# Performance work log

Measured on AMD Instinct MI355X. Metric: run time of the kernel, lower is better.

Reference implementation:

```python
import jax, jax.numpy as jnp
import numpy as np

B, N, H, L = 8, 256, 128, 3
NF, EF, TD, FH = 6, 15, 4, 64  # node feat, edge feat, temporal dim, flow hidden


def setup_inputs() -> dict:
    key = jax.random.key(0)
    ks = jax.random.split(key, 16)
    s = 0.05
    return {
        "node_features": jax.random.normal(ks[0], (B, N, NF), jnp.float32),
        "edge_features": jax.random.normal(ks[1], (B, N, N, EF), jnp.float32),
        "temporal_features": jax.random.normal(ks[2], (B, N, N, TD), jnp.float32),
        "adjacency": jax.random.randint(ks[3], (N, N), 0, 2, jnp.int32),
        "W_emb": jax.random.normal(ks[4], (NF, H), jnp.float32) * s,
        "b_emb": jnp.zeros((H,), jnp.float32),
        "msg_W": jax.random.normal(ks[5], (L, H + 3, H), jnp.float32) * s,
        "msg_b": jnp.zeros((L, H), jnp.float32),
        "upd_W": jax.random.normal(ks[6], (L, 2 * H, H), jnp.float32) * s,
        "upd_b": jnp.zeros((L, H), jnp.float32),
        "W1": jax.random.normal(ks[7], (2 * H + 3 + TD, FH), jnp.float32) * s,
        "b1": jnp.zeros((FH,), jnp.float32),
        "W2": jax.random.normal(ks[8], (FH, 1), jnp.float32) * s,
        "b2": jnp.zeros((1,), jnp.float32),
    }


def reference(node_features, edge_features, temporal_features, adjacency,
              W_emb, b_emb, msg_W, msg_b, upd_W, upd_b, W1, b1, W2, b2):
    # mask[j, i] = 1 if node i is a neighbor of node j (adjacency[j] > 0)
    mask = (adjacency > 0).astype(node_features.dtype)          # [N, N]
    deg = mask.sum(axis=1)                                      # [N]
    edge_rel = edge_features[..., -3:]                          # [B, N, N, 3]
    # aggregated relation features per destination j: sum_i mask[j,i] * edge_rel[b,i,j,:]
    r_agg = jnp.einsum('ji,bijc->bjc', mask, edge_rel)          # [B, N, 3]

    # node embedding (dropout = identity in eval)
    emb = jax.nn.relu(node_features @ W_emb + b_emb)            # [B, N, H]

    for l in range(L):
        We, Wr = msg_W[l, :H], msg_W[l, H:]                     # [H,H], [3,H]
        # msg_nn is linear, so the masked sum decomposes exactly:
        # messages[b,j] = sum_i mask[j,i]*(emb_i @ We + r_ij @ Wr + b)
        messages = (jnp.einsum('ji,bih->bjh', mask, emb @ We)
                    + r_agg @ Wr
                    + deg[None, :, None] * msg_b[l])            # [B, N, H]
        emb = jax.nn.relu(
            jnp.concatenate([emb, messages], axis=-1) @ upd_W[l] + upd_b[l])

    # pairwise flow MLP, first Linear split by input blocks [emb_i, emb_j, r, t]
    Wi, Wj = W1[:H], W1[H:2 * H]
    Wr1, Wt = W1[2 * H:2 * H + 3], W1[2 * H + 3:]
    hi = emb @ Wi                                               # [B, N, FH]
    hj = emb @ Wj                                               # [B, N, FH]
    h = jax.nn.relu(hi[:, :, None, :] + hj[:, None, :, :]
                    + edge_rel @ Wr1 + temporal_features @ Wt + b1)  # [B,N,N,FH]
    flows = jax.nn.relu(h @ W2 + b2)[..., 0]                    # [B, N, N]
    return flows
```

## Files before the change

kernel.cpp:

```cpp
#include <hip/hip_runtime.h>

#define B 8
#define N 256
#define H 128
#define NF 6
#define EF 15
#define TD 4
#define FH 64
#define M (B*N)

typedef unsigned short u16;
using short8  = __attribute__((ext_vector_type(8))) short;
using short4v = __attribute__((ext_vector_type(4))) short;
using f32x4   = __attribute__((ext_vector_type(4))) float;

__device__ __forceinline__ u16 f2bf(float x) {
    unsigned u = __float_as_uint(x);
    u += 0x7fffu + ((u >> 16) & 1u);
    return (u16)(u >> 16);
}
__device__ __forceinline__ float bf2f(u16 h) {
    return __uint_as_float(((unsigned)h) << 16);
}

__global__ __launch_bounds__(256) void k_setup(
    const float* __restrict__ edge, const int* __restrict__ adj,
    const float* __restrict__ nf, const float* __restrict__ Wemb,
    const float* __restrict__ bemb,
    const float* __restrict__ msg_W, const float* __restrict__ upd_W,
    const float* __restrict__ W1,
    float* __restrict__ e0p, float* __restrict__ e1p, float* __restrict__ e2p,
    float* __restrict__ rp0, float* __restrict__ rp1, float* __restrict__ rp2,
    float* __restrict__ deg,
    u16* __restrict__ WeTh, u16* __restrict__ WeTl,
    u16* __restrict__ UwTh, u16* __restrict__ UwTl,
    u16* __restrict__ W1Th, u16* __restrict__ W1Tl,
    u16* __restrict__ eRh, u16* __restrict__ eRl,
    u16* __restrict__ eTh, u16* __restrict__ eTl)
{
    __shared__ __align__(16) float smem[3848];
    __shared__ float red[4];
    const int t = threadIdx.x;
    const int blk = blockIdx.x;

    if (blk < 2048) {
        const int i = blk & 255;
        const float* src = edge + (size_t)blk * (N * EF);
        float4* s4 = (float4*)smem;
#pragma unroll
        for (int u = 0; u < 4; ++u) {
            int idx = t + u * 256;
            if (idx < (N * EF) / 4) s4[idx] = *(const float4*)(src + idx * 4);
        }
        __syncthreads();
        const int j = t;
        float e0 = smem[j * EF + 12];
        float e1 = smem[j * EF + 13];
        float e2 = smem[j * EF + 14];
        size_t base = (size_t)blk * N + j;
        e0p[base] = e0; e1p[base] = e1; e2p[base] = e2;
        float m = (adj[j * N + i] > 0) ? 1.f : 0.f;
        rp0[base] = m * e0; rp1[base] = m * e1; rp2[base] = m * e2;
    } else if (blk < 2688) {
        int idx = (blk - 2048) * 256 + t;
        float v; u16 *dh, *dl; int d;
        if (idx < 3 * 16384) {
            int l = idx / 16384, r = idx & 16383;
            int c = r >> 7, h = r & 127;
            v = msg_W[l * ((H + 3) * H) + h * H + c];
            dh = WeTh; dl = WeTl; d = idx;
        } else if (idx < 3 * 16384 + 3 * 32768) {
            int r0 = idx - 3 * 16384;
            int l = r0 / 32768, r = r0 & 32767;
            int c = r >> 8, k = r & 255;
            v = upd_W[l * (2 * H * H) + k * H + c];
            dh = UwTh; dl = UwTl; d = r0;
        } else {
            int r0 = idx - 3 * 16384 - 3 * 32768;
            int f = r0 >> 8, k = r0 & 255;
            v = W1[k * FH + f];
            dh = W1Th; dl = W1Tl; d = r0;
        }
        u16 h = f2bf(v);
        dh[d] = h;
        dl[d] = f2bf(v - bf2f(h));
    } else if (blk < 2816) {
        int tile = blk - 2688;
        float (*sout)[132] = (float(*)[132])smem;
        {
            int row = t >> 4, h0 = (t & 15) * 8;
            int gr = tile * 16 + row;
            float xv[NF];
#pragma unroll
            for (int k = 0; k < NF; ++k) xv[k] = nf[gr * NF + k];
#pragma unroll
            for (int c = 0; c < 8; ++c) {
                float a = bemb[h0 + c];
#pragma unroll
                for (int k = 0; k < NF; ++k) a += xv[k] * Wemb[k * H + h0 + c];
                sout[row][h0 + c] = fmaxf(a, 0.f);
            }
        }
        __syncthreads();
        {
            int row = t >> 4, h0 = (t & 15) * 8;
            int gr = tile * 16 + row;
            short8 ph, pl;
#pragma unroll
            for (int c = 0; c < 8; ++c) {
                float x = sout[row][h0 + c];
                u16 h = f2bf(x);
                ph[c] = (short)h;
                pl[c] = (short)f2bf(x - bf2f(h));
            }
            *(short8*)&eRh[(size_t)gr * H + h0] = ph;
            *(short8*)&eRl[(size_t)gr * H + h0] = pl;
        }
        {
            int hh = t >> 1, jj = (t & 1) * 8;
            short8 th, tl;
#pragma unroll
            for (int r = 0; r < 8; ++r) {
                float x = sout[jj + r][hh];
                u16 h = f2bf(x);
                th[r] = (short)h;
                tl[r] = (short)f2bf(x - bf2f(h));
            }
            size_t o = (size_t)(tile >> 4) * H * N + (size_t)hh * N + ((tile & 15) * 16) + jj;
            *(short8*)&eTh[o] = th;
            *(short8*)&eTl[o] = tl;
        }
    } else {
        int jr = blk - 2816;
        float v = (adj[jr * N + t] > 0) ? 1.f : 0.f;
        for (int o = 32; o > 0; o >>= 1) v += __shfl_down(v, o);
        if ((t & 63) == 0) red[t >> 6] = v;
        __syncthreads();
        if (t == 0) deg[jr] = red[0] + red[1] + red[2] + red[3];
    }
}

#define PIPE(NC, LD, COMP)                          \
    LD(0, pA0, pA1);                                \
    LD(1, pB0, pB1);                                \
    WRX(0, pA0, pA1);                               \
    __syncthreads();                                \
    _Pragma("unroll")                               \
    for (int c = 0; c < (NC); c += 2) {             \
        WRX(1, pB0, pB1);                           \
        if (c + 2 < (NC)) LD(c + 2, pA0, pA1);      \
        COMP(c, 0);                                 \
        __syncthreads();                            \
        if (c + 2 < (NC)) WRX(0, pA0, pA1);         \
        if (c + 3 < (NC)) LD(c + 3, pB0, pB1);      \
        COMP(c + 1, 1);                             \
        __syncthreads();                            \
    }

template <bool FIRST, bool LAST>
__global__ __launch_bounds__(512) void k_layer(
    const u16* __restrict__ embR_hi, const u16* __restrict__ embR_lo,
    const u16* __restrict__ embT_hi, const u16* __restrict__ embT_lo,
    const int* __restrict__ adj,
    const float* __restrict__ rp0, const float* __restrict__ rp1,
    const float* __restrict__ rp2, float* __restrict__ ragg,
    const float* __restrict__ deg,
    const u16* __restrict__ WeT_hi, const u16* __restrict__ WeT_lo,
    const float* __restrict__ mwl, const float* __restrict__ mbl,
    const u16* __restrict__ UwT_hi, const u16* __restrict__ UwT_lo,
    const float* __restrict__ ubl,
    u16* __restrict__ oR_hi, u16* __restrict__ oR_lo,
    u16* __restrict__ oT_hi, u16* __restrict__ oT_lo,
    const u16* __restrict__ W1T_hi, const u16* __restrict__ W1T_lo,
    float* __restrict__ hi_out, float* __restrict__ hj_out)
{
    __shared__ __align__(16) u16 sbt[2][2][128][40];
    __shared__ __align__(16) u16 smask[16][264];
    __shared__ __align__(16) u16 semb_hi[16][136], semb_lo[16][136];
    __shared__ __align__(16) u16 sagg_hi[16][136], sagg_lo[16][136];
    __shared__ __align__(16) u16 smsg_hi[16][136], smsg_lo[16][136];
    __shared__ __align__(16) float sout[16][132];
    __shared__ float sragg[16][4];

    const int t = threadIdx.x;
    const int wave = t >> 6, lane = t & 63;
    const int lrow = lane & 15;
    const int kg8  = (lane >> 4) * 8;
    const int rb   = (lane >> 4) * 4;
    const int cb   = wave * 16;
    const int blk  = blockIdx.x;
    const int b    = blk >> 4, tile = blk & 15;
    const int j0   = tile * 16;
    const int gb   = b * N;

    const int sp = t >> 8, task = t & 255;
    const int sh = task >> 2, sseg = (task & 3) * 8;

    short8 pA0, pA1, pB0, pB1;

    {
        int j = t >> 5, i0 = (t & 31) * 8;
        int4 a0 = *(const int4*)(adj + (j0 + j) * N + i0);
        int4 a1 = *(const int4*)(adj + (j0 + j) * N + i0 + 4);
        short8 mrow;
        mrow[0] = (a0.x > 0) ? (short)0x3F80 : (short)0;
        mrow[1] = (a0.y > 0) ? (short)0x3F80 : (short)0;
        mrow[2] = (a0.z > 0) ? (short)0x3F80 : (short)0;
        mrow[3] = (a0.w > 0) ? (short)0x3F80 : (short)0;
        mrow[4] = (a1.x > 0) ? (short)0x3F80 : (short)0;
        mrow[5] = (a1.y > 0) ? (short)0x3F80 : (short)0;
        mrow[6] = (a1.z > 0) ? (short)0x3F80 : (short)0;
        mrow[7] = (a1.w > 0) ? (short)0x3F80 : (short)0;
        *(short8*)&smask[j][i0] = mrow;
        int h0 = (t & 31) * 4;
        *(short4v*)&semb_hi[j][h0] = *(const short4v*)&embR_hi[(size_t)(gb + j0 + j) * H + h0];
        *(short4v*)&semb_lo[j][h0] = *(const short4v*)&embR_lo[(size_t)(gb + j0 + j) * H + h0];
    }

    if constexpr (FIRST) {
        int j16 = t >> 5, ic = t & 31;
        int gj = gb + j0 + j16;
        float s0 = 0.f, s1 = 0.f, s2 = 0.f;
#pragma unroll
        for (int k = 0; k < 8; ++k) {
            size_t o = ((size_t)(gb + ic * 8 + k)) * N + (j0 + j16);
            s0 += rp0[o]; s1 += rp1[o]; s2 += rp2[o];
        }
        for (int o = 16; o > 0; o >>= 1) {
            s0 += __shfl_down(s0, o, 32);
            s1 += __shfl_down(s1, o, 32);
            s2 += __shfl_down(s2, o, 32);
        }
        if (ic == 0) {
            sragg[j16][0] = s0; sragg[j16][1] = s1; sragg[j16][2] = s2;
            float* rg = ragg + (size_t)gj * 3;
            rg[0] = s0; rg[1] = s1; rg[2] = s2;
        }
    } else {
        if (t < 48) sragg[t / 3][t % 3] = ragg[(size_t)(gb + j0 + t / 3) * 3 + (t % 3)];
    }

    const u16* sA_hi = embT_hi + (size_t)b * H * N;
    const u16* sA_lo = embT_lo + (size_t)b * H * N;

#define WRX(buf, q0, q1)                              \
    { *(short8*)&sbt[buf][sp][sh][sseg] = q0;         \
      *(short8*)&sbt[buf][sp][sh + 64][sseg] = q1; }

#define LDA(c, q0, q1)                                                        \
    { const u16* s_ = sp ? sA_lo : sA_hi;                                     \
      q0 = *(const short8*)(s_ + (size_t)sh * N + (c) * 32 + sseg);           \
      q1 = *(const short8*)(s_ + (size_t)(sh + 64) * N + (c) * 32 + sseg); }

#define LDB(c, q0, q1)                                                        \
    { const u16* s_ = sp ? WeT_lo : WeT_hi;                                   \
      q0 = *(const short8*)(s_ + (size_t)sh * H + (c) * 32 + sseg);           \
      q1 = *(const short8*)(s_ + (size_t)(sh + 64) * H + (c) * 32 + sseg); }

#define LDC(c, q0, q1)                                                        \
    { const u16* s_ = sp ? UwT_lo : UwT_hi;                                   \
      q0 = *(const short8*)(s_ + (size_t)sh * 2 * H + (c) * 32 + sseg);       \
      q1 = *(const short8*)(s_ + (size_t)(sh + 64) * 2 * H + (c) * 32 + sseg); }

#define LDD(c, q0, q1)                                                        \
    { const u16* s_ = sp ? W1T_lo : W1T_hi;                                   \
      q0 = *(const short8*)(s_ + (size_t)sh * 256 + (c) * 32 + sseg);         \
      q1 = *(const short8*)(s_ + (size_t)sh * 256 + 128 + (c) * 32 + sseg); }

#define COMPA(c, buf)                                                           \
    { short8 am = *(const short8*)&smask[lrow][(c) * 32 + kg8];                 \
      short8 bh = *(const short8*)&sbt[buf][0][cb + lrow][kg8];                 \
      short8 bl = *(const short8*)&sbt[buf][1][cb + lrow][kg8];                 \
      acc = __builtin_amdgcn_mfma_f32_16x16x32_bf16(am, bh, acc, 0, 0, 0);      \
      acc = __builtin_amdgcn_mfma_f32_16x16x32_bf16(am, bl, acc, 0, 0, 0); }

#define COMPB(c, buf)                                                           \
    { short8 ah = *(const short8*)&sagg_hi[lrow][(c) * 32 + kg8];               \
      short8 al = *(const short8*)&sagg_lo[lrow][(c) * 32 + kg8];               \
      short8 bh = *(const short8*)&sbt[buf][0][cb + lrow][kg8];                 \
      short8 bl = *(const short8*)&sbt[buf][1][cb + lrow][kg8];                 \
      acc = __builtin_amdgcn_mfma_f32_16x16x32_bf16(ah, bh, acc, 0, 0, 0);      \
      acc = __builtin_amdgcn_mfma_f32_16x16x32_bf16(ah, bl, acc, 0, 0, 0);      \
      acc = __builtin_amdgcn_mfma_f32_16x16x32_bf16(al, bh, acc, 0, 0, 0); }

#define COMPC(c, buf)                                                           \
    { int kc = ((c) & 3) * 32 + kg8; short8 ah, al;                             \
      if ((c) < 4) { ah = *(const short8*)&semb_hi[lrow][kc];                   \
                     al = *(const short8*)&semb_lo[lrow][kc]; }                 \
      else         { ah = *(const short8*)&smsg_hi[lrow][kc];                   \
                     al = *(const short8*)&smsg_lo[lrow][kc]; }                 \
      short8 bh = *(const short8*)&sbt[buf][0][cb + lrow][kg8];                 \
      short8 bl = *(const short8*)&sbt[buf][1][cb + lrow][kg8];                 \
      acc = __builtin_amdgcn_mfma_f32_16x16x32_bf16(ah, bh, acc, 0, 0, 0);      \
      acc = __builtin_amdgcn_mfma_f32_16x16x32_bf16(ah, bl, acc, 0, 0, 0);      \
      acc = __builtin_amdgcn_mfma_f32_16x16x32_bf16(al, bh, acc, 0, 0, 0); }

#define COMPD(c, buf)                                                           \
    { short8 ah = *(const short8*)&sagg_hi[lrow][(c) * 32 + kg8];               \
      short8 al = *(const short8*)&sagg_lo[lrow][(c) * 32 + kg8];               \
      short8 bh = *(const short8*)&sbt[buf][0][br][kg8];                        \
      short8 bl = *(const short8*)&sbt[buf][1][br][kg8];                        \
      acc = __builtin_amdgcn_mfma_f32_16x16x32_bf16(ah, bh, acc, 0, 0, 0);      \
      acc = __builtin_amdgcn_mfma_f32_16x16x32_bf16(ah, bl, acc, 0, 0, 0);      \
      acc = __builtin_amdgcn_mfma_f32_16x16x32_bf16(al, bh, acc, 0, 0, 0); }

    f32x4 acc = {0.f, 0.f, 0.f, 0.f};
    PIPE(8, LDA, COMPA)
#pragma unroll
    for (int r = 0; r < 4; ++r) {
        float v = acc[r];
        u16 h = f2bf(v);
        sagg_hi[rb + r][cb + lrow] = h;
        sagg_lo[rb + r][cb + lrow] = f2bf(v - bf2f(h));
    }

    acc = (f32x4){0.f, 0.f, 0.f, 0.f};
    PIPE(4, LDB, COMPB)
    {
        int hp = cb + lrow;
        float w0 = mwl[(H + 0) * H + hp];
        float w1 = mwl[(H + 1) * H + hp];
        float w2 = mwl[(H + 2) * H + hp];
        float mb = mbl[hp];
#pragma unroll
        for (int r = 0; r < 4; ++r) {
            int jl = j0 + rb + r;
            float v = acc[r] + deg[jl] * mb
                    + sragg[rb + r][0] * w0 + sragg[rb + r][1] * w1
                    + sragg[rb + r][2] * w2;
            u16 h = f2bf(v);
            smsg_hi[rb + r][hp] = h;
            smsg_lo[rb + r][hp] = f2bf(v - bf2f(h));
        }
    }

    acc = (f32x4){0.f, 0.f, 0.f, 0.f};
    PIPE(8, LDC, COMPC)
    {
        float ub = ubl[cb + lrow];
#pragma unroll
        for (int r = 0; r < 4; ++r) {
            float v = fmaxf(acc[r] + ub, 0.f);
            if constexpr (LAST) {
                u16 h = f2bf(v);
                sagg_hi[rb + r][cb + lrow] = h;
                sagg_lo[rb + r][cb + lrow] = f2bf(v - bf2f(h));
            } else {
                sout[rb + r][cb + lrow] = v;
            }
        }
    }
    __syncthreads();

    if constexpr (!LAST) {
        {
            int row = t >> 5, h0 = (t & 31) * 4;
            int gr = gb + j0 + row;
            float4 v = *(const float4*)&sout[row][h0];
            float xs[4] = {v.x, v.y, v.z, v.w};
            short4v ph, pl;
#pragma unroll
            for (int c = 0; c < 4; ++c) {
                u16 h = f2bf(xs[c]);
                ph[c] = (short)h;
                pl[c] = (short)f2bf(xs[c] - bf2f(h));
            }
            *(short4v*)&oR_hi[(size_t)gr * H + h0] = ph;
            *(short4v*)&oR_lo[(size_t)gr * H + h0] = pl;
        }
        {
            int hh = t >> 2, jj = (t & 3) * 4;
            short4v th, tl;
#pragma unroll
            for (int r = 0; r < 4; ++r) {
                float x = sout[jj + r][hh];
                u16 h = f2bf(x);
                th[r] = (short)h;
                tl[r] = (short)f2bf(x - bf2f(h));
            }
            size_t o = (size_t)b * H * N + (size_t)hh * N + j0 + jj;
            *(short4v*)&oT_hi[o] = th;
            *(short4v*)&oT_lo[o] = tl;
        }
    } else {
        const int br = ((wave >= 4) ? 64 : 0) + (wave & 3) * 16 + lrow;
        acc = (f32x4){0.f, 0.f, 0.f, 0.f};
        PIPE(4, LDD, COMPD)
#pragma unroll
        for (int r = 0; r < 4; ++r) sout[rb + r][br] = acc[r];
        __syncthreads();
        int row = t >> 5, c0 = (t & 31) * 4;
        int gr = gb + j0 + row;
        float4 v = *(const float4*)&sout[row][c0];
        if (c0 < 64) *(float4*)&hi_out[(size_t)gr * FH + c0] = v;
        else         *(float4*)&hj_out[(size_t)gr * FH + (c0 - 64)] = v;
    }
#undef WRX
#undef LDA
#undef LDB
#undef LDC
#undef LDD
#undef COMPA
#undef COMPB
#undef COMPC
#undef COMPD
}

__global__ __launch_bounds__(256) void k_final(
    const float* __restrict__ hi, const float* __restrict__ hj,
    const float* __restrict__ e0p, const float* __restrict__ e1p,
    const float* __restrict__ e2p, const float* __restrict__ temporal,
    const float* __restrict__ W1, const float* __restrict__ b1,
    const float* __restrict__ W2, const float* __restrict__ b2,
    float* __restrict__ flows) {
    __shared__ float his[8][FH];
    __shared__ float hjs[32][FH + 2];
    __shared__ float wr0[FH], wr1[FH], wr2[FH];
    __shared__ float wt0[FH], wt1[FH], wt2[FH], wt3[FH], bb[FH], w2s[FH];
    int blk = blockIdx.x;
    int jt = blk & 7, it = (blk >> 3) & 31, b = blk >> 8;
    int tid = threadIdx.x;
#pragma unroll
    for (int u = 0; u < 2; ++u) {
        int idx = u * 256 + tid;
        his[idx >> 6][idx & 63] = hi[((size_t)(b * N) + it * 8 + (idx >> 6)) * FH + (idx & 63)];
    }
#pragma unroll
    for (int u = 0; u < 8; ++u) {
        int idx = u * 256 + tid;
        hjs[idx >> 6][idx & 63] = hj[((size_t)(b * N) + jt * 32 + (idx >> 6)) * FH + (idx & 63)];
    }
    {
        int f = tid & 63, g = tid >> 6;
        if (g == 0) { wr0[f] = W1[(2 * H + 0) * FH + f]; wt0[f] = W1[(2 * H + 3) * FH + f]; bb[f] = b1[f]; }
        if (g == 1) { wr1[f] = W1[(2 * H + 1) * FH + f]; wt1[f] = W1[(2 * H + 4) * FH + f]; w2s[f] = W2[f]; }
        if (g == 2) { wr2[f] = W1[(2 * H + 2) * FH + f]; wt2[f] = W1[(2 * H + 5) * FH + f]; }
        if (g == 3) { wt3[f] = W1[(2 * H + 6) * FH + f]; }
    }
    __syncthreads();
    int ti = tid >> 5, tj = tid & 31;
    int i = it * 8 + ti, j = jt * 32 + tj;
    size_t pij = ((size_t)(b * N) + i) * N + j;
    float e0 = e0p[pij], e1 = e1p[pij], e2 = e2p[pij];
    float4 tf = *(const float4*)(temporal + pij * TD);
    float acc = 0.f;
#pragma unroll 8
    for (int f = 0; f < FH; ++f) {
        float v = his[ti][f] + hjs[tj][f] + bb[f]
                + e0 * wr0[f] + e1 * wr1[f] + e2 * wr2[f]
                + tf.x * wt0[f] + tf.y * wt1[f] + tf.z * wt2[f] + tf.w * wt3[f];
        acc += fmaxf(v, 0.f) * w2s[f];
    }
    flows[pij] = fmaxf(acc + b2[0], 0.f);
}

extern "C" void kernel_launch(void* const* d_in, const int* in_sizes, int n_in,
                              void* d_out, int out_size, void* d_ws, size_t ws_size,
                              hipStream_t stream) {
    const float* nf       = (const float*)d_in[0];
    const float* edge     = (const float*)d_in[1];
    const float* temporal = (const float*)d_in[2];
    const int*   adj      = (const int*)d_in[3];
    const float* W_emb    = (const float*)d_in[4];
    const float* b_emb    = (const float*)d_in[5];
    const float* msg_W    = (const float*)d_in[6];
    const float* msg_b    = (const float*)d_in[7];
    const float* upd_W    = (const float*)d_in[8];
    const float* upd_b    = (const float*)d_in[9];
    const float* W1       = (const float*)d_in[10];
    const float* b1       = (const float*)d_in[11];
    const float* W2       = (const float*)d_in[12];
    const float* b2       = (const float*)d_in[13];
    float* out = (float*)d_out;
    (void)in_sizes; (void)n_in; (void)out_size; (void)ws_size;

    char* p = (char*)d_ws;
    auto take = [&](size_t bytes) { char* r = p; p += (bytes + 255) & ~(size_t)255; return r; };
    float* deg   = (float*)take(256 * 4);
    float* ragg  = (float*)take((size_t)M * 3 * 4);
    float* e0p   = (float*)take((size_t)B * N * N * 4);
    float* e1p   = (float*)take((size_t)B * N * N * 4);
    float* e2p   = (float*)take((size_t)B * N * N * 4);
    float* rp0   = (float*)take((size_t)B * N * N * 4);
    float* rp1   = (float*)take((size_t)B * N * N * 4);
    float* rp2   = (float*)take((size_t)B * N * N * 4);
    float* hi    = (float*)take((size_t)M * FH * 4);
    float* hj    = (float*)take((size_t)M * FH * 4);
    u16* eRhA = (u16*)take((size_t)M * H * 2);
    u16* eRlA = (u16*)take((size_t)M * H * 2);
    u16* eThA = (u16*)take((size_t)M * H * 2);
    u16* eTlA = (u16*)take((size_t)M * H * 2);
    u16* eRhB = (u16*)take((size_t)M * H * 2);
    u16* eRlB = (u16*)take((size_t)M * H * 2);
    u16* eThB = (u16*)take((size_t)M * H * 2);
    u16* eTlB = (u16*)take((size_t)M * H * 2);
    u16* WeTh = (u16*)take(3 * 16384 * 2);
    u16* WeTl = (u16*)take(3 * 16384 * 2);
    u16* UwTh = (u16*)take(3 * 32768 * 2);
    u16* UwTl = (u16*)take(3 * 32768 * 2);
    u16* W1Th = (u16*)take(16384 * 2);
    u16* W1Tl = (u16*)take(16384 * 2);

    k_setup<<<3072, 256, 0, stream>>>(edge, adj, nf, W_emb, b_emb,
                                      msg_W, upd_W, W1,
                                      e0p, e1p, e2p, rp0, rp1, rp2, deg,
                                      WeTh, WeTl, UwTh, UwTl, W1Th, W1Tl,
                                      eRhA, eRlA, eThA, eTlA);

    const int mwS = (H + 3) * H;
    k_layer<true, false><<<128, 512, 0, stream>>>(
        eRhA, eRlA, eThA, eTlA, adj, rp0, rp1, rp2, ragg, deg,
        WeTh + 0 * 16384, WeTl + 0 * 16384, msg_W + 0 * mwS, msg_b + 0 * H,
        UwTh + 0 * 32768, UwTl + 0 * 32768, upd_b + 0 * H,
        eRhB, eRlB, eThB, eTlB, W1Th, W1Tl, hi, hj);
    k_layer<false, false><<<128, 512, 0, stream>>>(
        eRhB, eRlB, eThB, eTlB, adj, rp0, rp1, rp2, ragg, deg,
        WeTh + 1 * 16384, WeTl + 1 * 16384, msg_W + 1 * mwS, msg_b + 1 * H,
        UwTh + 1 * 32768, UwTl + 1 * 32768, upd_b + 1 * H,
        eRhA, eRlA, eThA, eTlA, W1Th, W1Tl, hi, hj);
    k_layer<false, true><<<128, 512, 0, stream>>>(
        eRhA, eRlA, eThA, eTlA, adj, rp0, rp1, rp2, ragg, deg,
        WeTh + 2 * 16384, WeTl + 2 * 16384, msg_W + 2 * mwS, msg_b + 2 * H,
        UwTh + 2 * 32768, UwTl + 2 * 32768, upd_b + 2 * H,
        eRhB, eRlB, eThB, eTlB, W1Th, W1Tl, hi, hj);

    k_final<<<2048, 256, 0, stream>>>(hi, hj, e0p, e1p, e2p, temporal,
                                      W1, b1, W2, b2, out);
}
```

Measured before the change: 73.78 us.

## Load MFMA B operands directly from global memory instead of LDS double-buffering

Removes the shared-memory double-buffered staging pipeline for the B operands in the layer kernel. Each wave now loads its hi/lo B fragments straight from global memory into registers inside unrolled loops. This drops the many __syncthreads barriers and LDS round-trips per chunk and frees about 40KB of LDS, which may raise occupancy. In exchange it depends on cache hits for operands that are reused across waves and blocks, and the global loads are no longer overlapped with compute through explicit prefetch.

Measured after the change: 83.13 us. +12.7%, slower.

```diff
diff --git a/kernel.cpp b/kernel.cpp
--- a/kernel.cpp
+++ b/kernel.cpp
@@ -140,23 +140,6 @@
     }
 }
 
-#define PIPE(NC, LD, COMP)                          \
-    LD(0, pA0, pA1);                                \
-    LD(1, pB0, pB1);                                \
-    WRX(0, pA0, pA1);                               \
-    __syncthreads();                                \
-    _Pragma("unroll")                               \
-    for (int c = 0; c < (NC); c += 2) {             \
-        WRX(1, pB0, pB1);                           \
-        if (c + 2 < (NC)) LD(c + 2, pA0, pA1);      \
-        COMP(c, 0);                                 \
-        __syncthreads();                            \
-        if (c + 2 < (NC)) WRX(0, pA0, pA1);         \
-        if (c + 3 < (NC)) LD(c + 3, pB0, pB1);      \
-        COMP(c + 1, 1);                             \
-        __syncthreads();                            \
-    }
-
 template <bool FIRST, bool LAST>
 __global__ __launch_bounds__(512) void k_layer(
     const u16* __restrict__ embR_hi, const u16* __restrict__ embR_lo,
@@ -174,7 +157,6 @@
     const u16* __restrict__ W1T_hi, const u16* __restrict__ W1T_lo,
     float* __restrict__ hi_out, float* __restrict__ hj_out)
 {
-    __shared__ __align__(16) u16 sbt[2][2][128][40];
     __shared__ __align__(16) u16 smask[16][264];
     __shared__ __align__(16) u16 semb_hi[16][136], semb_lo[16][136];
     __shared__ __align__(16) u16 sagg_hi[16][136], sagg_lo[16][136];
@@ -192,11 +174,6 @@
     const int b    = blk >> 4, tile = blk & 15;
     const int j0   = tile * 16;
     const int gb   = b * N;
-
-    const int sp = t >> 8, task = t & 255;
-    const int sh = task >> 2, sseg = (task & 3) * 8;
-
-    short8 pA0, pA1, pB0, pB1;
 
     {
         int j = t >> 5, i0 = (t & 31) * 8;
@@ -239,73 +216,21 @@
     } else {
         if (t < 48) sragg[t / 3][t % 3] = ragg[(size_t)(gb + j0 + t / 3) * 3 + (t % 3)];
     }
-
-    const u16* sA_hi = embT_hi + (size_t)b * H * N;
-    const u16* sA_lo = embT_lo + (size_t)b * H * N;
-
-#define WRX(buf, q0, q1)                              \
-    { *(short8*)&sbt[buf][sp][sh][sseg] = q0;         \
-      *(short8*)&sbt[buf][sp][sh + 64][sseg] = q1; }
-
-#define LDA(c, q0, q1)                                                        \
-    { const u16* s_ = sp ? sA_lo : sA_hi;                                     \
-      q0 = *(const short8*)(s_ + (size_t)sh * N + (c) * 32 + sseg);           \
-      q1 = *(const short8*)(s_ + (size_t)(sh + 64) * N + (c) * 32 + sseg); }
-
-#define LDB(c, q0, q1)                                                        \
-    { const u16* s_ = sp ? WeT_lo : WeT_hi;                                   \
-      q0 = *(const short8*)(s_ + (size_t)sh * H + (c) * 32 + sseg);           \
-      q1 = *(const short8*)(s_ + (size_t)(sh + 64) * H + (c) * 32 + sseg); }
-
-#define LDC(c, q0, q1)                                                        \
-    { const u16* s_ = sp ? UwT_lo : UwT_hi;                                   \
-      q0 = *(const short8*)(s_ + (size_t)sh * 2 * H + (c) * 32 + sseg);       \
-      q1 = *(const short8*)(s_ + (size_t)(sh + 64) * 2 * H + (c) * 32 + sseg); }
-
-#define LDD(c, q0, q1)                                                        \
-    { const u16* s_ = sp ? W1T_lo : W1T_hi;                                   \
-      q0 = *(const short8*)(s_ + (size_t)sh * 256 + (c) * 32 + sseg);         \
-      q1 = *(const short8*)(s_ + (size_t)sh * 256 + 128 + (c) * 32 + sseg); }
-
-#define COMPA(c, buf)                                                           \
-    { short8 am = *(const short8*)&smask[lrow][(c) * 32 + kg8];                 \
-      short8 bh = *(const short8*)&sbt[buf][0][cb + lrow][kg8];                 \
-      short8 bl = *(const short8*)&sbt[buf][1][cb + lrow][kg8];                 \
-      acc = __builtin_amdgcn_mfma_f32_16x16x32_bf16(am, bh, acc, 0, 0, 0);      \
-      acc = __builtin_amdgcn_mfma_f32_16x16x32_bf16(am, bl, acc, 0, 0, 0); }
-
-#define COMPB(c, buf)                                                           \
-    { short8 ah = *(const short8*)&sagg_hi[lrow][(c) * 32 + kg8];               \
-      short8 al = *(const short8*)&sagg_lo[lrow][(c) * 32 + kg8];               \
-      short8 bh = *(const short8*)&sbt[buf][0][cb + lrow][kg8];                 \
-      short8 bl = *(const short8*)&sbt[buf][1][cb + lrow][kg8];                 \
-      acc = __builtin_amdgcn_mfma_f32_16x16x32_bf16(ah, bh, acc, 0, 0, 0);      \
-      acc = __builtin_amdgcn_mfma_f32_16x16x32_bf16(ah, bl, acc, 0, 0, 0);      \
-      acc = __builtin_amdgcn_mfma_f32_16x16x32_bf16(al, bh, acc, 0, 0, 0); }
-
-#define COMPC(c, buf)                                                           \
-    { int kc = ((c) & 3) * 32 + kg8; short8 ah, al;                             \
-      if ((c) < 4) { ah = *(const short8*)&semb_hi[lrow][kc];                   \
-                     al = *(const short8*)&semb_lo[lrow][kc]; }                 \
-      else         { ah = *(const short8*)&smsg_hi[lrow][kc];                   \
-                     al = *(const short8*)&smsg_lo[lrow][kc]; }                 \
-      short8 bh = *(const short8*)&sbt[buf][0][cb + lrow][kg8];                 \
-      short8 bl = *(const short8*)&sbt[buf][1][cb + lrow][kg8];                 \
-      acc = __builtin_amdgcn_mfma_f32_16x16x32_bf16(ah, bh, acc, 0, 0, 0);      \
-      acc = __builtin_amdgcn_mfma_f32_16x16x32_bf16(ah, bl, acc, 0, 0, 0);      \
-      acc = __builtin_amdgcn_mfma_f32_16x16x32_bf16(al, bh, acc, 0, 0, 0); }
-
-#define COMPD(c, buf)                                                           \
-    { short8 ah = *(const short8*)&sagg_hi[lrow][(c) * 32 + kg8];               \
-      short8 al = *(const short8*)&sagg_lo[lrow][(c) * 32 + kg8];               \
-      short8 bh = *(const short8*)&sbt[buf][0][br][kg8];                        \
-      short8 bl = *(const short8*)&sbt[buf][1][br][kg8];                        \
-      acc = __builtin_amdgcn_mfma_f32_16x16x32_bf16(ah, bh, acc, 0, 0, 0);      \
-      acc = __builtin_amdgcn_mfma_f32_16x16x32_bf16(ah, bl, acc, 0, 0, 0);      \
-      acc = __builtin_amdgcn_mfma_f32_16x16x32_bf16(al, bh, acc, 0, 0, 0); }
+    __syncthreads();
 
     f32x4 acc = {0.f, 0.f, 0.f, 0.f};
-    PIPE(8, LDA, COMPA)
+    {
+        const u16* bhp = embT_hi + (size_t)b * H * N + (size_t)(cb + lrow) * N;
+        const u16* blp = embT_lo + (size_t)b * H * N + (size_t)(cb + lrow) * N;
+#pragma unroll
+        for (int c = 0; c < 8; ++c) {
+            short8 bh = *(const short8*)(bhp + c * 32 + kg8);
+            short8 bl = *(const short8*)(blp + c * 32 + kg8);
+            short8 am = *(const short8*)&smask[lrow][c * 32 + kg8];
+            acc = __builtin_amdgcn_mfma_f32_16x16x32_bf16(am, bh, acc, 0, 0, 0);
+            acc = __builtin_amdgcn_mfma_f32_16x16x32_bf16(am, bl, acc, 0, 0, 0);
+        }
+    }
 #pragma unroll
     for (int r = 0; r < 4; ++r) {
         float v = acc[r];
@@ -313,9 +238,23 @@
         sagg_hi[rb + r][cb + lrow] = h;
         sagg_lo[rb + r][cb + lrow] = f2bf(v - bf2f(h));
     }
+    __syncthreads();
 
     acc = (f32x4){0.f, 0.f, 0.f, 0.f};
-    PIPE(4, LDB, COMPB)
+    {
+        const u16* bhp = WeT_hi + (size_t)(cb + lrow) * H;
+        const u16* blp = WeT_lo + (size_t)(cb + lrow) * H;
+#pragma unroll
+        for (int c = 0; c < 4; ++c) {
+            short8 bh = *(const short8*)(bhp + c * 32 + kg8);
+            short8 bl = *(const short8*)(blp + c * 32 + kg8);
+            short8 ah = *(const short8*)&sagg_hi[lrow][c * 32 + kg8];
+            short8 al = *(const short8*)&sagg_lo[lrow][c * 32 + kg8];
+            acc = __builtin_amdgcn_mfma_f32_16x16x32_bf16(ah, bh, acc, 0, 0, 0);
+            acc = __builtin_amdgcn_mfma_f32_16x16x32_bf16(ah, bl, acc, 0, 0, 0);
+            acc = __builtin_amdgcn_mfma_f32_16x16x32_bf16(al, bh, acc, 0, 0, 0);
+        }
+    }
     {
         int hp = cb + lrow;
         float w0 = mwl[(H + 0) * H + hp];
@@ -333,9 +272,30 @@
             smsg_lo[rb + r][hp] = f2bf(v - bf2f(h));
         }
     }
+    __syncthreads();
 
     acc = (f32x4){0.f, 0.f, 0.f, 0.f};
-    PIPE(8, LDC, COMPC)
+    {
+        const u16* bhp = UwT_hi + (size_t)(cb + lrow) * (2 * H);
+        const u16* blp = UwT_lo + (size_t)(cb + lrow) * (2 * H);
+#pragma unroll
+        for (int c = 0; c < 8; ++c) {
+            short8 bh = *(const short8*)(bhp + c * 32 + kg8);
+            short8 bl = *(const short8*)(blp + c * 32 + kg8);
+            int kc = (c & 3) * 32 + kg8;
+            short8 ah, al;
+            if (c < 4) {
+                ah = *(const short8*)&semb_hi[lrow][kc];
+                al = *(const short8*)&semb_lo[lrow][kc];
+            } else {
+                ah = *(const short8*)&smsg_hi[lrow][kc];
+                al = *(const short8*)&smsg_lo[lrow][kc];
+            }
+            acc = __builtin_amdgcn_mfma_f32_16x16x32_bf16(ah, bh, acc, 0, 0, 0);
+            acc = __builtin_amdgcn_mfma_f32_16x16x32_bf16(ah, bl, acc, 0, 0, 0);
+            acc = __builtin_amdgcn_mfma_f32_16x16x32_bf16(al, bh, acc, 0, 0, 0);
+        }
+    }
     {
         float ub = ubl[cb + lrow];
 #pragma unroll
@@ -383,11 +343,26 @@
             *(short4v*)&oT_lo[o] = tl;
         }
     } else {
-        const int br = ((wave >= 4) ? 64 : 0) + (wave & 3) * 16 + lrow;
+        const int fD   = (wave & 3) * 16 + lrow;
+        const int koD  = (wave >= 4) ? 128 : 0;
+        const int colD = ((wave >= 4) ? 64 : 0) + fD;
         acc = (f32x4){0.f, 0.f, 0.f, 0.f};
-        PIPE(4, LDD, COMPD)
-#pragma unroll
-        for (int r = 0; r < 4; ++r) sout[rb + r][br] = acc[r];
+        {
+            const u16* bhp = W1T_hi + (size_t)fD * 256 + koD;
+            const u16* blp = W1T_lo + (size_t)fD * 256 + koD;
+#pragma unroll
+            for (int c = 0; c < 4; ++c) {
+                short8 bh = *(const short8*)(bhp + c * 32 + kg8);
+                short8 bl = *(const short8*)(blp + c * 32 + kg8);
+                short8 ah = *(const short8*)&sagg_hi[lrow][c * 32 + kg8];
+                short8 al = *(const short8*)&sagg_lo[lrow][c * 32 + kg8];
+                acc = __builtin_amdgcn_mfma_f32_16x16x32_bf16(ah, bh, acc, 0, 0, 0);
+                acc = __builtin_amdgcn_mfma_f32_16x16x32_bf16(ah, bl, acc, 0, 0, 0);
+                acc = __builtin_amdgcn_mfma_f32_16x16x32_bf16(al, bh, acc, 0, 0, 0);
+            }
+        }
+#pragma unroll
+        for (int r = 0; r < 4; ++r) sout[rb + r][colD] = acc[r];
         __syncthreads();
         int row = t >> 5, c0 = (t & 31) * 4;
         int gr = gb + j0 + row;
@@ -395,15 +370,6 @@
         if (c0 < 64) *(float4*)&hi_out[(size_t)gr * FH + c0] = v;
         else         *(float4*)&hj_out[(size_t)gr * FH + (c0 - 64)] = v;
     }
-#undef WRX
-#undef LDA
-#undef LDB
-#undef LDC
-#undef LDD
-#undef COMPA
-#undef COMPB
-#undef COMPC
-#undef COMPD
 }
 
 __global__ __launch_bounds__(256) void k_final(
```
